# Kernel tuning notes

Measured on AMD Instinct MI355X. Metric: run time of the kernel, lower is better.

Reference implementation:

```python
import jax, jax.numpy as jnp
import numpy as np

MARGIN = 1.0
ALFA = 0.1


def setup_inputs() -> dict:
    key = jax.random.key(0)
    k1, k2 = jax.random.split(key)
    N, D, T = 262144, 128, 262144
    embeddings = jax.random.normal(k1, (N, D), dtype=jnp.float32)
    triplets = jax.random.randint(k2, (T, 3), 0, N, dtype=jnp.int64)
    return {"embeddings": embeddings, "triplets": triplets}


def _corr_loss(embeddings):
    # torch_cov(rowvar=False): columns are variables -> D x D covariance
    N, D = embeddings.shape
    m = embeddings - jnp.mean(embeddings, axis=0, keepdims=True)  # [N, D]
    cov = jnp.einsum('ni,nj->ij', m, m) / (N - 1)                 # [D, D]
    V = jnp.diagonal(cov)                                          # variances
    corr2 = (cov / jnp.sqrt(V[:, None] * V[None, :])) ** 2
    # strict lower triangle, n*(n-1)/2 elements, then mean
    tril = jnp.tril(jnp.ones((D, D), dtype=corr2.dtype), k=-1)
    return jnp.sum(corr2 * tril) / (D * (D - 1) / 2)


def _triplet_loss(embeddings, triplets):
    pivot = embeddings[triplets[:, 0]]
    positives = embeddings[triplets[:, 1]]
    negatives = embeddings[triplets[:, 2]]
    ap = jnp.sum((pivot - positives) ** 2, axis=1)
    an = jnp.sum((pivot - negatives) ** 2, axis=1)
    return jnp.mean(jax.nn.relu(ap - an + MARGIN))


def reference(embeddings, triplets):
    corr_loss = _corr_loss(embeddings)
    triplet_loss = _triplet_loss(embeddings, triplets)
    return triplet_loss + ALFA * corr_loss
```

## Files before the change

### kernel.cpp

```cpp
#include <hip/hip_runtime.h>

#define D 128
#define MARGIN 1.0f
#define ALFA 0.1f
#define KC 64
#define GB 512

#define WS_TSUM   0
#define WS_GRAM   256
#define WS_COLSUM (WS_GRAM + D * D)
#define WS_ZERO   (WS_COLSUM + D)
#define WS_PART   16896
#define PART_STRIDE (D * D + D)
#define WS_TAB_F  (WS_PART + GB * PART_STRIDE)

typedef __attribute__((ext_vector_type(8)))  short bf16x8;
typedef __attribute__((ext_vector_type(8)))  unsigned short u16x8;
typedef __attribute__((ext_vector_type(16))) float f32x16;

__device__ __forceinline__ unsigned short f2bf(float f) {
    unsigned u = __float_as_uint(f);
    u += 0x7FFFu + ((u >> 16) & 1u);
    return (unsigned short)(u >> 16);
}
__device__ __forceinline__ float bf2f(unsigned short u) {
    return __uint_as_float((unsigned)u << 16);
}

__global__ __launch_bounds__(512, 4) void gram_mfma_write(const float* __restrict__ emb,
                                                          int rowsPerBlock,
                                                          float* __restrict__ ws,
                                                          unsigned short* __restrict__ tab) {
    __shared__ __align__(16) char lds[2][128 * 128];
    __shared__ float csred[D];

    const int tid = threadIdx.x;
    const int l   = tid & 63;
    const int w   = tid >> 6;
    const int r0  = blockIdx.x * rowsPerBlock;

    const int rT = w & 3;
    const int c0 = (w >> 2) * 2;

    f32x16 acc0 = {};
    f32x16 acc1 = {};
    float cs[4] = {0.f, 0.f, 0.f, 0.f};
    const int d0 = (tid & 31) * 4;

    auto stage = [&](int cc, int b) {
#pragma unroll
        for (int j = 0; j < 2; ++j) {
            const int k = j * 32 + (tid >> 5) * 2;
            const int rowg = r0 + cc * KC + k;
            const float* base = emb + (size_t)rowg * D + d0;
            float4 a  = *(const float4*)base;
            float4 bv = *(const float4*)(base + D);
            ushort4 ua, ub;
            unsigned short* pa = (unsigned short*)&ua;
            unsigned short* pb = (unsigned short*)&ub;
#pragma unroll
            for (int i = 0; i < 4; ++i) {
                float av = ((const float*)&a)[i];
                float bb = ((const float*)&bv)[i];
                cs[i] += av + bb;
                unsigned short ha = f2bf(av), hb = f2bf(bb);
                pa[i] = ha; pb[i] = hb;
                unsigned slotp = (unsigned)(k >> 3) ^ (unsigned)((tid & 31) & 7);
                unsigned off = (unsigned)(d0 + i) * 128u + slotp * 16u + (unsigned)((k & 7) << 1);
                *(unsigned*)(&lds[b][off]) = (unsigned)ha | ((unsigned)hb << 16);
            }
            *(ushort4*)&tab[(size_t)rowg * D + d0]       = ua;
            *(ushort4*)&tab[(size_t)(rowg + 1) * D + d0] = ub;
        }
    };

    auto frag = [&](int t, int kb, int b) -> bf16x8 {
        const int d = t * 32 + (l & 31);
        const int k = kb + (l >> 5) * 8;
        unsigned slotp = (unsigned)(k >> 3) ^ ((unsigned)(d >> 2) & 7u);
        return *(const bf16x8*)(&lds[b][(unsigned)d * 128u + slotp * 16u]);
    };

    const int nChunks = rowsPerBlock / KC;
    stage(0, 0);
    for (int cc = 0; cc < nChunks; ++cc) {
        const int b = cc & 1;
        __syncthreads();
        if (cc + 1 < nChunks) stage(cc + 1, b ^ 1);
#pragma unroll
        for (int kb = 0; kb < KC; kb += 16) {
            bf16x8 fr = frag(rT,     kb, b);
            bf16x8 f0 = frag(c0,     kb, b);
            bf16x8 f1 = frag(c0 + 1, kb, b);
            acc0 = __builtin_amdgcn_mfma_f32_32x32x16_bf16(fr, f0, acc0, 0, 0, 0);
            acc1 = __builtin_amdgcn_mfma_f32_32x32x16_bf16(fr, f1, acc1, 0, 0, 0);
        }
    }
    __syncthreads();

    if (tid < D) csred[tid] = 0.f;
    __syncthreads();
#pragma unroll
    for (int i = 0; i < 4; ++i) atomicAdd(&csred[d0 + i], cs[i]);
    __syncthreads();

    float* gram   = ws + WS_PART + (size_t)blockIdx.x * PART_STRIDE;
    float* colsum = gram + D * D;

    if (tid < D) colsum[tid] = csred[tid];

    const int row_hi = (l >> 5) * 4;
    const int col    = l & 31;
#pragma unroll
    for (int reg = 0; reg < 16; ++reg) {
        const int row32 = (reg & 3) + 8 * (reg >> 2) + row_hi;
        const int gr    = (rT * 32 + row32) * D;
        gram[gr + c0 * 32 + col]       = acc0[reg];
        gram[gr + (c0 + 1) * 32 + col] = acc1[reg];
    }
}

__global__ __launch_bounds__(256) void triplet_bf16(const unsigned short* __restrict__ tab,
                                                    const int* __restrict__ trip,
                                                    int T,
                                                    float* __restrict__ ws) {
    const int tid = threadIdx.x;
    const int li  = tid & 15;
    const int grp = (blockIdx.x * 256 + tid) >> 4;
    const int NG  = (gridDim.x * 256) >> 4;

    float wsum = 0.f;

    for (int t0 = grp; t0 < T; t0 += 4 * NG) {
        u16x8 P[4], Q[4], R[4];
#pragma unroll
        for (int u = 0; u < 4; ++u) {
            const int t = t0 + u * NG;
            if (t < T) {
                const int i0 = trip[3 * t], i1 = trip[3 * t + 1], i2 = trip[3 * t + 2];
                P[u] = *(const u16x8*)&tab[(size_t)i0 * D + li * 8];
                Q[u] = *(const u16x8*)&tab[(size_t)i1 * D + li * 8];
                R[u] = *(const u16x8*)&tab[(size_t)i2 * D + li * 8];
            }
        }
#pragma unroll
        for (int u = 0; u < 4; ++u) {
            const int t = t0 + u * NG;
            if (t < T) {
                float s = 0.f;
#pragma unroll
                for (int e = 0; e < 8; ++e) {
                    float p = bf2f(P[u][e]);
                    float dp = p - bf2f(Q[u][e]);
                    float dn = p - bf2f(R[u][e]);
                    s += dp * dp - dn * dn;
                }
#pragma unroll
                for (int off = 8; off; off >>= 1) s += __shfl_xor(s, off, 64);
                if (li == 0) wsum += fmaxf(s + MARGIN, 0.f);
            }
        }
    }

    __shared__ float red[16];
    if (li == 0) red[tid >> 4] = wsum;
    __syncthreads();
    if (tid == 0) {
        float b = 0.f;
#pragma unroll
        for (int i = 0; i < 16; ++i) b += red[i];
        atomicAdd(&ws[WS_TSUM], b);
    }
}

__global__ __launch_bounds__(256) void reduce_partials(float* __restrict__ ws, int P, int slices) {
    const int nIdxBlocks = (PART_STRIDE + 255) / 256;
    const int idx   = (blockIdx.x % nIdxBlocks) * 256 + threadIdx.x;
    const int slice = blockIdx.x / nIdxBlocks;
    if (idx >= PART_STRIDE) return;
    const int per = P / slices;
    const float* part = ws + WS_PART;
    float s = 0.f;
    const int p0 = slice * per;
#pragma unroll 8
    for (int p = 0; p < per; ++p)
        s += part[(size_t)(p0 + p) * PART_STRIDE + idx];
    if (idx < D * D) atomicAdd(&ws[WS_GRAM + idx], s);
    else             atomicAdd(&ws[WS_COLSUM + (idx - D * D)], s);
}

__global__ __launch_bounds__(256) void finalize_kernel(const float* __restrict__ ws,
                                                       float* __restrict__ out,
                                                       int N, int T) {
    const float* gram   = ws + WS_GRAM;
    const float* colsum = ws + WS_COLSUM;

    __shared__ float V[D];
    __shared__ float red[256];

    const int tid = threadIdx.x;
    const float invN   = 1.0f / (float)N;
    const float invNm1 = 1.0f / (float)(N - 1);

    if (tid < D) {
        float m = colsum[tid] * invN;
        V[tid] = (gram[tid * D + tid] - (float)N * m * m) * invNm1;
    }
    __syncthreads();

    float local = 0.f;
    for (int idx = tid; idx < D * D; idx += 256) {
        int i = idx >> 7, j = idx & 127;
        if (j < i) {
            float mi  = colsum[i] * invN;
            float mj  = colsum[j] * invN;
            float cov = (gram[idx] - (float)N * mi * mj) * invNm1;
            local += cov * cov / (V[i] * V[j]);
        }
    }
    red[tid] = local;
    __syncthreads();
    for (int s = 128; s > 0; s >>= 1) {
        if (tid < s) red[tid] += red[tid + s];
        __syncthreads();
    }
    if (tid == 0) {
        float corr_mean = red[0] / ((float)D * (float)(D - 1) * 0.5f);
        out[0] = ws[WS_TSUM] / (float)T + ALFA * corr_mean;
    }
}

__device__ __forceinline__ float d2diff(float4 p, float4 q, float4 r) {
    float ax = p.x - q.x, ay = p.y - q.y, az = p.z - q.z, aw = p.w - q.w;
    float bx = p.x - r.x, by = p.y - r.y, bz = p.z - r.z, bw = p.w - r.w;
    return (ax * ax + ay * ay + az * az + aw * aw)
         - (bx * bx + by * by + bz * bz + bw * bw);
}

__global__ __launch_bounds__(512, 4) void fused_fallback(const float* __restrict__ emb,
                                                         const int* __restrict__ trip,
                                                         int rowsPerBlock, int T,
                                                         float* __restrict__ ws) {
    __shared__ __align__(16) char lds[2][128 * 128];
    __shared__ float csred[D];
    const int tid = threadIdx.x;

    if (blockIdx.x < GB) {
        const int l = tid & 63, w = tid >> 6, r0 = blockIdx.x * rowsPerBlock;
        const int rT = w & 3, c0 = (w >> 2) * 2;
        f32x16 acc0 = {}, acc1 = {};
        float cs[4] = {0.f, 0.f, 0.f, 0.f};
        const int d0 = (tid & 31) * 4;

        auto stage = [&](int cc, int b) {
#pragma unroll
            for (int j = 0; j < 2; ++j) {
                const int k = j * 32 + (tid >> 5) * 2;
                const float* base = emb + (size_t)(r0 + cc * KC + k) * D + d0;
                float4 a = *(const float4*)base;
                float4 bv = *(const float4*)(base + D);
#pragma unroll
                for (int i = 0; i < 4; ++i) {
                    float av = ((const float*)&a)[i], bb = ((const float*)&bv)[i];
                    cs[i] += av + bb;
                    unsigned slotp = (unsigned)(k >> 3) ^ (unsigned)((tid & 31) & 7);
                    unsigned off = (unsigned)(d0 + i) * 128u + slotp * 16u + (unsigned)((k & 7) << 1);
                    *(unsigned*)(&lds[b][off]) = (unsigned)f2bf(av) | ((unsigned)f2bf(bb) << 16);
                }
            }
        };
        auto frag = [&](int t, int kb, int b) -> bf16x8 {
            const int d = t * 32 + (l & 31);
            const int k = kb + (l >> 5) * 8;
            unsigned slotp = (unsigned)(k >> 3) ^ ((unsigned)(d >> 2) & 7u);
            return *(const bf16x8*)(&lds[b][(unsigned)d * 128u + slotp * 16u]);
        };
        const int nChunks = rowsPerBlock / KC;
        stage(0, 0);
        for (int cc = 0; cc < nChunks; ++cc) {
            const int b = cc & 1;
            __syncthreads();
            if (cc + 1 < nChunks) stage(cc + 1, b ^ 1);
#pragma unroll
            for (int kb = 0; kb < KC; kb += 16) {
                bf16x8 fr = frag(rT, kb, b);
                bf16x8 f0 = frag(c0, kb, b);
                bf16x8 f1 = frag(c0 + 1, kb, b);
                acc0 = __builtin_amdgcn_mfma_f32_32x32x16_bf16(fr, f0, acc0, 0, 0, 0);
                acc1 = __builtin_amdgcn_mfma_f32_32x32x16_bf16(fr, f1, acc1, 0, 0, 0);
            }
        }
        __syncthreads();
        if (tid < D) csred[tid] = 0.f;
        __syncthreads();
#pragma unroll
        for (int i = 0; i < 4; ++i) atomicAdd(&csred[d0 + i], cs[i]);
        __syncthreads();
        if (tid < D) atomicAdd(&ws[WS_COLSUM + tid], csred[tid]);
        const int row_hi = (l >> 5) * 4, col = l & 31;
#pragma unroll
        for (int reg = 0; reg < 16; ++reg) {
            const int row32 = (reg & 3) + 8 * (reg >> 2) + row_hi;
            const int gr = (rT * 32 + row32) * D;
            atomicAdd(&ws[WS_GRAM + gr + c0 * 32 + col], acc0[reg]);
            atomicAdd(&ws[WS_GRAM + gr + (c0 + 1) * 32 + col], acc1[reg]);
        }
    } else {
        const int li = tid & 31, hwl = tid >> 5;
        const int hw = (blockIdx.x - GB) * 16 + hwl;
        const int NH = 1024 * 16;
        float wsum = 0.f;
        for (int t0 = hw; t0 < T; t0 += 4 * NH) {
            float4 P[4], Q[4], R[4];
#pragma unroll
            for (int k = 0; k < 4; ++k) {
                const int t = t0 + k * NH;
                if (t < T) {
                    const int i0 = trip[3 * t], i1 = trip[3 * t + 1], i2 = trip[3 * t + 2];
                    P[k] = ((const float4*)(emb + (size_t)i0 * D))[li];
                    Q[k] = ((const float4*)(emb + (size_t)i1 * D))[li];
                    R[k] = ((const float4*)(emb + (size_t)i2 * D))[li];
                }
            }
#pragma unroll
            for (int k = 0; k < 4; ++k) {
                const int t = t0 + k * NH;
                if (t < T) {
                    float s = d2diff(P[k], Q[k], R[k]);
#pragma unroll
                    for (int off = 16; off; off >>= 1) s += __shfl_xor(s, off, 64);
                    if (li == 0) wsum += fmaxf(s + MARGIN, 0.f);
                }
            }
        }
        if (li == 0) csred[hwl] = wsum;
        __syncthreads();
        if (tid == 0) {
            float b = 0.f;
#pragma unroll
            for (int i = 0; i < 16; ++i) b += csred[i];
            atomicAdd(&ws[WS_TSUM], b);
        }
    }
}

extern "C" void kernel_launch(void* const* d_in, const int* in_sizes, int n_in,
                              void* d_out, int out_size, void* d_ws, size_t ws_size,
                              hipStream_t stream) {
    const float* emb  = (const float*)d_in[0];
    const int*   trip = (const int*)d_in[1];
    float*       out  = (float*)d_out;
    float*       ws   = (float*)d_ws;

    const int N = in_sizes[0] / D;
    const int T = in_sizes[1] / 3;

    hipMemsetAsync(d_ws, 0, WS_ZERO * sizeof(float), stream);

    const size_t needB = (size_t)WS_TAB_F * 4 + (size_t)N * D * 2;

    if (ws_size >= needB) {
        unsigned short* tab = (unsigned short*)(ws + WS_TAB_F);
        gram_mfma_write<<<GB, 512, 0, stream>>>(emb, N / GB, ws, tab);
        triplet_bf16<<<1024, 256, 0, stream>>>(tab, trip, T, ws);
        reduce_partials<<<65 * 16, 256, 0, stream>>>(ws, GB, 16);
    } else {
        fused_fallback<<<GB + 1024, 512, 0, stream>>>(emb, trip, N / GB, T, ws);
    }

    finalize_kernel<<<1, 256, 0, stream>>>(ws, out, N, T);
}
```

Baseline: 276.9 us.

## Merge partial reduction into triplet kernel and double Gram grid with smaller chunks

The Gram kernel now runs 1024 blocks with 32-row chunks and a halved LDS buffer using a 4-way swizzle, which should raise occupancy and spread the conversion and table-write work. The separate reduce_partials launch is folded into the triplet kernel as extra leading blocks, removing one launch and letting the reduction overlap with the gathers. The triplet gather is unrolled to 6 triplets in flight per group over 2048 blocks to raise memory-level parallelism. In exchange, twice as many Gram partials must be reduced, and register pressure in the triplet kernel grows.

```diff
diff --git a/kernel.cpp b/kernel.cpp
--- a/kernel.cpp
+++ b/kernel.cpp
@@ -3,7 +3,10 @@
 #define D 128
 #define MARGIN 1.0f
 #define ALFA 0.1f
-#define KC 64
+#define KC 32
+#define GRAMB 1024
+#define RBLK 520
+#define TB 2048
 #define GB 512
 
 #define WS_TSUM   0
@@ -12,7 +15,7 @@
 #define WS_ZERO   (WS_COLSUM + D)
 #define WS_PART   16896
 #define PART_STRIDE (D * D + D)
-#define WS_TAB_F  (WS_PART + GB * PART_STRIDE)
+#define WS_TAB_F  (WS_PART + GRAMB * PART_STRIDE)
 
 typedef __attribute__((ext_vector_type(8)))  short bf16x8;
 typedef __attribute__((ext_vector_type(8)))  unsigned short u16x8;
@@ -31,7 +34,7 @@
                                                           int rowsPerBlock,
                                                           float* __restrict__ ws,
                                                           unsigned short* __restrict__ tab) {
-    __shared__ __align__(16) char lds[2][128 * 128];
+    __shared__ __align__(16) char lds[2][128 * 64];
     __shared__ float csred[D];
 
     const int tid = threadIdx.x;
@@ -46,39 +49,36 @@
     f32x16 acc1 = {};
     float cs[4] = {0.f, 0.f, 0.f, 0.f};
     const int d0 = (tid & 31) * 4;
+    const int ks = (tid >> 5) * 2;
 
     auto stage = [&](int cc, int b) {
-#pragma unroll
-        for (int j = 0; j < 2; ++j) {
-            const int k = j * 32 + (tid >> 5) * 2;
-            const int rowg = r0 + cc * KC + k;
-            const float* base = emb + (size_t)rowg * D + d0;
-            float4 a  = *(const float4*)base;
-            float4 bv = *(const float4*)(base + D);
-            ushort4 ua, ub;
-            unsigned short* pa = (unsigned short*)&ua;
-            unsigned short* pb = (unsigned short*)&ub;
-#pragma unroll
-            for (int i = 0; i < 4; ++i) {
-                float av = ((const float*)&a)[i];
-                float bb = ((const float*)&bv)[i];
-                cs[i] += av + bb;
-                unsigned short ha = f2bf(av), hb = f2bf(bb);
-                pa[i] = ha; pb[i] = hb;
-                unsigned slotp = (unsigned)(k >> 3) ^ (unsigned)((tid & 31) & 7);
-                unsigned off = (unsigned)(d0 + i) * 128u + slotp * 16u + (unsigned)((k & 7) << 1);
-                *(unsigned*)(&lds[b][off]) = (unsigned)ha | ((unsigned)hb << 16);
-            }
-            *(ushort4*)&tab[(size_t)rowg * D + d0]       = ua;
-            *(ushort4*)&tab[(size_t)(rowg + 1) * D + d0] = ub;
-        }
+        const int rowg = r0 + cc * KC + ks;
+        const float* base = emb + (size_t)rowg * D + d0;
+        float4 a  = *(const float4*)base;
+        float4 bv = *(const float4*)(base + D);
+        ushort4 ua, ub;
+        unsigned short* pa = (unsigned short*)&ua;
+        unsigned short* pb = (unsigned short*)&ub;
+#pragma unroll
+        for (int i = 0; i < 4; ++i) {
+            float av = ((const float*)&a)[i];
+            float bb = ((const float*)&bv)[i];
+            cs[i] += av + bb;
+            unsigned short ha = f2bf(av), hb = f2bf(bb);
+            pa[i] = ha; pb[i] = hb;
+            unsigned slotp = (unsigned)(ks >> 3) ^ ((unsigned)((d0 + i) >> 2) & 3u);
+            unsigned off = (unsigned)(d0 + i) * 64u + slotp * 16u + (unsigned)((ks & 7) << 1);
+            *(unsigned*)(&lds[b][off]) = (unsigned)ha | ((unsigned)hb << 16);
+        }
+        *(ushort4*)&tab[(size_t)rowg * D + d0]       = ua;
+        *(ushort4*)&tab[(size_t)(rowg + 1) * D + d0] = ub;
     };
 
     auto frag = [&](int t, int kb, int b) -> bf16x8 {
         const int d = t * 32 + (l & 31);
         const int k = kb + (l >> 5) * 8;
-        unsigned slotp = (unsigned)(k >> 3) ^ ((unsigned)(d >> 2) & 7u);
-        return *(const bf16x8*)(&lds[b][(unsigned)d * 128u + slotp * 16u]);
+        unsigned slotp = (unsigned)(k >> 3) ^ ((unsigned)(d >> 2) & 3u);
+        return *(const bf16x8*)(&lds[b][(unsigned)d * 64u + slotp * 16u]);
     };
 
     const int nChunks = rowsPerBlock / KC;
@@ -120,21 +120,39 @@
     }
 }
 
-__global__ __launch_bounds__(256) void triplet_bf16(const unsigned short* __restrict__ tab,
-                                                    const int* __restrict__ trip,
-                                                    int T,
-                                                    float* __restrict__ ws) {
+__global__ __launch_bounds__(256) void triplet_red(const unsigned short* __restrict__ tab,
+                                                   const int* __restrict__ trip,
+                                                   int T,
+                                                   float* __restrict__ ws) {
+    __shared__ float red[16];
     const int tid = threadIdx.x;
+
+    if (blockIdx.x < RBLK) {
+        const int idx   = (blockIdx.x % 65) * 256 + tid;
+        const int slice = blockIdx.x / 65;
+        if (idx >= PART_STRIDE) return;
+        const int per = GRAMB / 8;
+        const float* part = ws + WS_PART;
+        float s = 0.f;
+        const int p0 = slice * per;
+#pragma unroll 8
+        for (int p = 0; p < per; ++p)
+            s += part[(size_t)(p0 + p) * PART_STRIDE + idx];
+        if (idx < D * D) atomicAdd(&ws[WS_GRAM + idx], s);
+        else             atomicAdd(&ws[WS_COLSUM + (idx - D * D)], s);
+        return;
+    }
+
     const int li  = tid & 15;
-    const int grp = (blockIdx.x * 256 + tid) >> 4;
-    const int NG  = (gridDim.x * 256) >> 4;
+    const int grp = ((blockIdx.x - RBLK) * 256 + tid) >> 4;
+    const int NG  = (TB * 256) >> 4;
 
     float wsum = 0.f;
 
-    for (int t0 = grp; t0 < T; t0 += 4 * NG) {
-        u16x8 P[4], Q[4], R[4];
-#pragma unroll
-        for (int u = 0; u < 4; ++u) {
+    for (int t0 = grp; t0 < T; t0 += 6 * NG) {
+        u16x8 P[6], Q[6], R[6];
+#pragma unroll
+        for (int u = 0; u < 6; ++u) {
             const int t = t0 + u * NG;
             if (t < T) {
                 const int i0 = trip[3 * t], i1 = trip[3 * t + 1], i2 = trip[3 * t + 2];
@@ -144,13 +162,13 @@
             }
         }
 #pragma unroll
-        for (int u = 0; u < 4; ++u) {
+        for (int u = 0; u < 6; ++u) {
             const int t = t0 + u * NG;
             if (t < T) {
                 float s = 0.f;
 #pragma unroll
                 for (int e = 0; e < 8; ++e) {
-                    float p = bf2f(P[u][e]);
+                    float p  = bf2f(P[u][e]);
                     float dp = p - bf2f(Q[u][e]);
                     float dn = p - bf2f(R[u][e]);
                     s += dp * dp - dn * dn;
@@ -162,7 +180,6 @@
         }
     }
 
-    __shared__ float red[16];
     if (li == 0) red[tid >> 4] = wsum;
     __syncthreads();
     if (tid == 0) {
@@ -171,22 +188,6 @@
         for (int i = 0; i < 16; ++i) b += red[i];
         atomicAdd(&ws[WS_TSUM], b);
     }
-}
-
-__global__ __launch_bounds__(256) void reduce_partials(float* __restrict__ ws, int P, int slices) {
-    const int nIdxBlocks = (PART_STRIDE + 255) / 256;
-    const int idx   = (blockIdx.x % nIdxBlocks) * 256 + threadIdx.x;
-    const int slice = blockIdx.x / nIdxBlocks;
-    if (idx >= PART_STRIDE) return;
-    const int per = P / slices;
-    const float* part = ws + WS_PART;
-    float s = 0.f;
-    const int p0 = slice * per;
-#pragma unroll 8
-    for (int p = 0; p < per; ++p)
-        s += part[(size_t)(p0 + p) * PART_STRIDE + idx];
-    if (idx < D * D) atomicAdd(&ws[WS_GRAM + idx], s);
-    else             atomicAdd(&ws[WS_COLSUM + (idx - D * D)], s);
 }
 
 __global__ __launch_bounds__(256) void finalize_kernel(const float* __restrict__ ws,
@@ -256,7 +257,7 @@
 #pragma unroll
             for (int j = 0; j < 2; ++j) {
                 const int k = j * 32 + (tid >> 5) * 2;
-                const float* base = emb + (size_t)(r0 + cc * KC + k) * D + d0;
+                const float* base = emb + (size_t)(r0 + cc * 64 + k) * D + d0;
                 float4 a = *(const float4*)base;
                 float4 bv = *(const float4*)(base + D);
 #pragma unroll
@@ -275,14 +276,14 @@
             unsigned slotp = (unsigned)(k >> 3) ^ ((unsigned)(d >> 2) & 7u);
             return *(const bf16x8*)(&lds[b][(unsigned)d * 128u + slotp * 16u]);
         };
-        const int nChunks = rowsPerBlock / KC;
+        const int nChunks = rowsPerBlock / 64;
         stage(0, 0);
         for (int cc = 0; cc < nChunks; ++cc) {
             const int b = cc & 1;
             __syncthreads();
             if (cc + 1 < nChunks) stage(cc + 1, b ^ 1);
 #pragma unroll
-            for (int kb = 0; kb < KC; kb += 16) {
+            for (int kb = 0; kb < 64; kb += 16) {
                 bf16x8 fr = frag(rT, kb, b);
                 bf16x8 f0 = frag(c0, kb, b);
                 bf16x8 f1 = frag(c0 + 1, kb, b);
@@ -361,9 +362,8 @@
 
     if (ws_size >= needB) {
         unsigned short* tab = (unsigned short*)(ws + WS_TAB_F);
-        gram_mfma_write<<<GB, 512, 0, stream>>>(emb, N / GB, ws, tab);
-        triplet_bf16<<<1024, 256, 0, stream>>>(tab, trip, T, ws);
-        reduce_partials<<<65 * 16, 256, 0, stream>>>(ws, GB, 16);
+        gram_mfma_write<<<GRAMB, 512, 0, stream>>>(emb, N / GRAMB, ws, tab);
+        triplet_red<<<RBLK + TB, 256, 0, stream>>>(tab, trip, T, ws);
     } else {
         fused_fallback<<<GB + 1024, 512, 0, stream>>>(emb, trip, N / GB, T, ws);
     }
```

New measurement: 292.4 us. 1.06x slower.
